# Kernel tuning notes

Measured on AMD Instinct MI355X. Metric: run time of the kernel, lower is better.

The kernel has to match this reference:

```python
import jax, jax.numpy as jnp
import numpy as np

NUM_STUDENTS = 50000
NUM_PROBLEMS = 10000
EMBED_DIM = 64
NNZ = 3200000


def _spmm(rows, cols, vals, x, num_out):
    # out[r] = sum_{edges e with rows[e]==r} vals[e] * x[cols[e]]
    msgs = vals[:, None] * x[cols]  # [nnz, d]
    return jax.ops.segment_sum(msgs, rows, num_segments=num_out)


def setup_inputs() -> dict:
    key = jax.random.key(0)
    ks = jax.random.split(key, 8)
    return {
        "student_embeds": jax.random.normal(ks[0], (NUM_STUDENTS, EMBED_DIM), jnp.float32),
        "problem_embeds": jax.random.normal(ks[1], (NUM_PROBLEMS, EMBED_DIM), jnp.float32),
        "a_rows": jax.random.randint(ks[2], (NNZ,), 0, NUM_STUDENTS, jnp.int32),
        "a_cols": jax.random.randint(ks[3], (NNZ,), 0, NUM_PROBLEMS, jnp.int32),
        "a_vals": jax.random.uniform(ks[4], (NNZ,), jnp.float32),
        "ia_rows": jax.random.randint(ks[5], (NNZ,), 0, NUM_STUDENTS, jnp.int32),
        "ia_cols": jax.random.randint(ks[6], (NNZ,), 0, NUM_PROBLEMS, jnp.int32),
        "ia_vals": jax.random.uniform(ks[7], (NNZ,), jnp.float32),
    }


def reference(student_embeds, problem_embeds, a_rows, a_cols, a_vals,
              ia_rows, ia_cols, ia_vals):
    num_students = student_embeds.shape[0]
    num_problems = problem_embeds.shape[0]
    # a_matrix @ problem_embeds
    student_embeds_c = _spmm(a_rows, a_cols, a_vals, problem_embeds, num_students)
    # a_matrix.T @ student_embeds (swap roles of rows/cols)
    problem_embeds_c = _spmm(a_cols, a_rows, a_vals, student_embeds, num_problems)
    student_embeds_ic = _spmm(ia_rows, ia_cols, ia_vals, problem_embeds, num_students)
    problem_embeds_ic = _spmm(ia_cols, ia_rows, ia_vals, student_embeds, num_problems)
    return (student_embeds_c, student_embeds_ic, problem_embeds_c, problem_embeds_ic)
```

## Files before the change

kernel.cpp:

```cpp
#include <hip/hip_runtime.h>
#include <hip/hip_bf16.h>

#define NBMAX 256
#define TILE  4096
#define KPT   16
#define BINSMAX 512
#define SLP   520

__device__ __forceinline__ int seg8(unsigned r, unsigned mult8) {
    return (int)__umulhi(r, mult8);
}

__global__ __launch_bounds__(256) void hist_all(
        const int* __restrict__ k0, const int* __restrict__ k1,
        const int* __restrict__ k2, const int* __restrict__ k3,
        int* __restrict__ gcnt4, int nnz, int rsh_s, int rsh_p) {
    __shared__ int h[NBMAX];
    int dir = blockIdx.x & 3;
    const int* key = (dir == 0) ? k0 : (dir == 1) ? k1 : (dir == 2) ? k2 : k3;
    int rsh = (dir & 1) ? rsh_p : rsh_s;
    h[threadIdx.x] = 0;
    __syncthreads();
    int ch = blockIdx.x >> 2, nch = gridDim.x >> 2;
    int nnz4 = nnz >> 2;
    for (int i = ch * 256 + threadIdx.x; i < nnz4; i += nch * 256) {
        int4 k4 = ((const int4*)key)[i];
        atomicAdd(&h[k4.x >> rsh], 1);
        atomicAdd(&h[k4.y >> rsh], 1);
        atomicAdd(&h[k4.z >> rsh], 1);
        atomicAdd(&h[k4.w >> rsh], 1);
    }
    if (ch == 0) {
        for (int i = (nnz4 << 2) + threadIdx.x; i < nnz; i += 256)
            atomicAdd(&h[key[i] >> rsh], 1);
    }
    __syncthreads();
    int v = h[threadIdx.x];
    if (v) atomicAdd(&gcnt4[dir * NBMAX + threadIdx.x], v);
}

__global__ __launch_bounds__(256) void scan_all(
        const int* __restrict__ gcnt4, int* __restrict__ boffs4,
        int* __restrict__ bcur4, int nb_s, int nb_p, int nnz,
        int* __restrict__ offsE, int* __restrict__ offsO, int NS, int NP8) {
    __shared__ int tmp[NBMAX];
    int dir = blockIdx.x, tid = threadIdx.x;
    int nb = (dir & 1) ? nb_p : nb_s;
    int v = (tid < nb) ? gcnt4[dir * NBMAX + tid] : 0;
    tmp[tid] = v;
    __syncthreads();
    for (int off = 1; off < NBMAX; off <<= 1) {
        int t = (tid >= off) ? tmp[tid - off] : 0;
        __syncthreads();
        tmp[tid] += t;
        __syncthreads();
    }
    if (tid < nb) {
        int e = tmp[tid] - v;
        boffs4[dir * (NBMAX + 1) + tid] = e;
        bcur4[dir * NBMAX + tid] = e;
    }
    if (tid == 0) boffs4[dir * (NBMAX + 1) + nb] = nnz;
    if (dir == 0 && tid == 0) { offsE[NS] = nnz; offsO[NP8] = nnz; }
}

__global__ __launch_bounds__(256) void staged_scatter(
        const int* __restrict__ key, const int* __restrict__ other,
        const float* __restrict__ vals, int* __restrict__ cursor,
        uint2* __restrict__ edges, int nnz, int rsh) {
    __shared__ int lhist[NBMAX], lofs[NBMAX], lbase[NBMAX];
    __shared__ uint2 stage[TILE];
    __shared__ int   sslot[TILE];
    int tid = threadIdx.x;
    int lmask = (1 << rsh) - 1;
    int ntiles = (nnz + TILE - 1) / TILE;
    for (int tile = blockIdx.x; tile < ntiles; tile += gridDim.x) {
        int tbeg = tile * TILE;
        int n = nnz - tbeg; if (n > TILE) n = TILE;
        lhist[tid] = 0;
        __syncthreads();
        int myb[KPT], myr[KPT]; unsigned myo[KPT]; float myv[KPT];
        #pragma unroll
        for (int g = 0; g < 4; ++g) {
            int s = g * 1024 + tid * 4;
            if (s + 4 <= n) {
                int i = tbeg + s;
                int4   k4 = *(const int4*)(key + i);
                int4   o4 = *(const int4*)(other + i);
                float4 v4 = *(const float4*)(vals + i);
                int   kk[4] = {k4.x, k4.y, k4.z, k4.w};
                int   oo[4] = {o4.x, o4.y, o4.z, o4.w};
                float vv[4] = {v4.x, v4.y, v4.z, v4.w};
                #pragma unroll
                for (int k = 0; k < 4; ++k) {
                    int m = g * 4 + k;
                    myb[m] = kk[k] >> rsh;
                    myo[m] = (unsigned)oo[k] | ((unsigned)(kk[k] & lmask) << 16);
                    myv[m] = vv[k];
                    myr[m] = atomicAdd(&lhist[myb[m]], 1);
                }
            } else {
                #pragma unroll
                for (int k = 0; k < 4; ++k) {
                    int m = g * 4 + k;
                    int s2 = s + k;
                    if (s2 < n) {
                        int i = tbeg + s2;
                        int ky = key[i];
                        myb[m] = ky >> rsh;
                        myo[m] = (unsigned)other[i] | ((unsigned)(ky & lmask) << 16);
                        myv[m] = vals[i];
                        myr[m] = atomicAdd(&lhist[myb[m]], 1);
                    } else myb[m] = -1;
                }
            }
        }
        __syncthreads();
        int h = lhist[tid];
        lofs[tid] = h;
        __syncthreads();
        for (int off = 1; off < NBMAX; off <<= 1) {
            int t = (tid >= off) ? lofs[tid - off] : 0;
            __syncthreads();
            lofs[tid] += t;
            __syncthreads();
        }
        lofs[tid] -= h;
        if (h > 0) lbase[tid] = atomicAdd(&cursor[tid], h);
        __syncthreads();
        #pragma unroll
        for (int k = 0; k < KPT; ++k) {
            if (myb[k] >= 0) {
                int ls = lofs[myb[k]] + myr[k];
                stage[ls] = make_uint2(myo[k], __float_as_uint(myv[k]));
                sslot[ls] = lbase[myb[k]] + myr[k];
            }
        }
        __syncthreads();
        #pragma unroll
        for (int k = 0; k < KPT; ++k) {
            int s = k * 256 + tid;
            if (s < n) edges[sslot[s]] = stage[s];
        }
        __syncthreads();
    }
}

__global__ __launch_bounds__(512) void row_scatter2(
        const uint2* __restrict__ e1, uint2* __restrict__ e2,
        const int* __restrict__ boffs, int* __restrict__ offs,
        int odd, int nb, int rsh, int nrows, unsigned mult8) {
    __shared__ int cnt[8 * SLP];
    __shared__ int tot[512];
    __shared__ int lcur[BINSMAX];
    int tid = threadIdx.x;
    int g = blockIdx.x;
    int x = g & 7;
    int sk = (g >> 3) & 7;
    int bi = g >> 6;
    int b = x + 8 * bi;
    if (b >= nb) return;
    int bins = odd ? (8 << rsh) : (1 << rsh);
    int beg = boffs[b], end = boffs[b + 1];
    int len = end - beg;
    for (int i = tid; i < 8 * SLP; i += 512) cnt[i] = 0;
    __syncthreads();
    int psh = 0;
    {
        int per = (len + 7) >> 3;
        while ((1 << psh) < per) psh++;
    }
    if (len > 0) {
        for (int i = beg + tid; i < end; i += 512) {
            uint2 e = e1[i];
            int lrow = (int)(e.x >> 16);
            int bin = odd ? (lrow * 8 + seg8(e.x & 0xFFFFu, mult8)) : lrow;
            int sl = (i - beg) >> psh;
            atomicAdd(&cnt[sl * SLP + bin], 1);
        }
    }
    __syncthreads();
    int own = 0;
    if (tid < bins) {
        #pragma unroll
        for (int j = 0; j < 8; ++j) own += cnt[j * SLP + tid];
    }
    tot[tid] = (tid < bins) ? own : 0;
    __syncthreads();
    for (int off = 1; off < 512; off <<= 1) {
        int t = (tid >= off) ? tot[tid - off] : 0;
        __syncthreads();
        tot[tid] += t;
        __syncthreads();
    }
    if (tid < bins) {
        int fineoff = tot[tid] - own;
        int basej = 0;
        for (int j = 0; j < sk; ++j) basej += cnt[j * SLP + tid];
        lcur[tid] = beg + fineoff + basej;
        if (sk == 0) {
            if (!odd) {
                int row = (b << rsh) + tid;
                if (row < nrows) offs[row] = beg + fineoff;
            } else {
                int row = (b << rsh) + (tid >> 3);
                if (row < nrows) offs[(row << 3) + (tid & 7)] = beg + fineoff;
            }
        }
    }
    __syncthreads();
    int lo = beg + (sk << psh);
    int hi = lo + (1 << psh); if (hi > end) hi = end;
    for (int i = lo + tid; i < hi; i += 512) {
        uint2 e = e1[i];
        int lrow = (int)(e.x >> 16);
        int bin = odd ? (lrow * 8 + seg8(e.x & 0xFFFFu, mult8)) : lrow;
        int slot = atomicAdd(&lcur[bin], 1);
        e2[slot] = make_uint2(e.x & 0xFFFFu, e.y);
    }
}

__device__ __forceinline__ float4 gather_row4(
        int beg, int end, const uint2* __restrict__ edges,
        const float* __restrict__ x, int lane) {
    int q = lane >> 4, l16 = lane & 15;
    const float* xq = x + (l16 << 2);
    float4 acc = make_float4(0.f, 0.f, 0.f, 0.f);
    for (int base = beg; base < end; base += 64) {
        int n = end - base; if (n > 64) n = 64;
        uint2 e = make_uint2(0u, 0u);
        if (lane < n) e = edges[base + lane];
        int   c0 = __shfl((int)e.x, q);
        float v0 = __uint_as_float(__shfl((int)e.y, q));
        int   c1 = __shfl((int)e.x, 4 + q);
        float v1 = __uint_as_float(__shfl((int)e.y, 4 + q));
        float4 x0 = *(const float4*)(xq + (((size_t)c0) << 6));
        float4 x1 = *(const float4*)(xq + (((size_t)c1) << 6));
        for (int j = 8; j < n; j += 8) {
            int   nc0 = __shfl((int)e.x, j + q);
            float nv0 = __uint_as_float(__shfl((int)e.y, j + q));
            int   nc1 = __shfl((int)e.x, j + 4 + q);
            float nv1 = __uint_as_float(__shfl((int)e.y, j + 4 + q));
            float4 nx0 = *(const float4*)(xq + (((size_t)nc0) << 6));
            float4 nx1 = *(const float4*)(xq + (((size_t)nc1) << 6));
            acc.x += v0 * x0.x; acc.y += v0 * x0.y;
            acc.z += v0 * x0.z; acc.w += v0 * x0.w;
            acc.x += v1 * x1.x; acc.y += v1 * x1.y;
            acc.z += v1 * x1.z; acc.w += v1 * x1.w;
            v0 = nv0; v1 = nv1; x0 = nx0; x1 = nx1;
        }
        acc.x += v0 * x0.x; acc.y += v0 * x0.y;
        acc.z += v0 * x0.z; acc.w += v0 * x0.w;
        acc.x += v1 * x1.x; acc.y += v1 * x1.y;
        acc.z += v1 * x1.z; acc.w += v1 * x1.w;
    }
    acc.x += __shfl_xor(acc.x, 16); acc.y += __shfl_xor(acc.y, 16);
    acc.z += __shfl_xor(acc.z, 16); acc.w += __shfl_xor(acc.w, 16);
    acc.x += __shfl_xor(acc.x, 32); acc.y += __shfl_xor(acc.y, 32);
    acc.z += __shfl_xor(acc.z, 32); acc.w += __shfl_xor(acc.w, 32);
    return acc;
}

__global__ __launch_bounds__(256) void row_gather(
        const int* __restrict__ offs, const uint2* __restrict__ edges,
        const float* __restrict__ x, float* __restrict__ out, int nrows) {
    int r = blockIdx.x * 4 + (threadIdx.x >> 6);
    int lane = threadIdx.x & 63;
    if (r >= nrows) return;
    float4 acc = gather_row4(offs[r], offs[r + 1], edges, x, lane);
    if ((lane >> 4) == 0)
        *(float4*)(out + (((size_t)r) << 6) + ((lane & 15) << 2)) = acc;
}

__global__ __launch_bounds__(256) void xcd_gather(
        const int* __restrict__ offs, const uint2* __restrict__ edges,
        const float* __restrict__ x, float* __restrict__ partial, int NP) {
    int g = blockIdx.x;
    int slot = g & 7;
    int t = g >> 3;
    int wave = threadIdx.x >> 6, lane = threadIdx.x & 63;
    int r = t * 4 + wave;
    if (r >= NP) return;
    int bin = r * 8 + slot;
    float4 acc = gather_row4(offs[bin], offs[bin + 1], edges, x, lane);
    if ((lane >> 4) == 0)
        *(float4*)(partial + (size_t)slot * NP * 64 + (((size_t)r) << 6) + ((lane & 15) << 2)) = acc;
}

__global__ __launch_bounds__(256) void reduce8(
        const float* __restrict__ partial, float* __restrict__ out, int n4) {
    int i = blockIdx.x * 256 + threadIdx.x;
    if (i < n4) {
        const float4* p = (const float4*)partial;
        float4 s = make_float4(0.f, 0.f, 0.f, 0.f);
        #pragma unroll
        for (int xx = 0; xx < 8; ++xx) {
            float4 v = p[(size_t)xx * n4 + i];
            s.x += v.x; s.y += v.y; s.z += v.z; s.w += v.w;
        }
        ((float4*)out)[i] = s;
    }
}

__global__ void spmm_scatter_kernel(const int* __restrict__ rows, const int* __restrict__ cols,
                                    const float* __restrict__ vals,
                                    const float* __restrict__ s_emb, const float* __restrict__ p_emb,
                                    float* __restrict__ out_s, float* __restrict__ out_p, int nnz) {
    long long t = (long long)blockIdx.x * blockDim.x + threadIdx.x;
    int e = (int)(t >> 6);
    int d = (int)(t & 63);
    if (e >= nnz) return;
    int r = rows[e];
    int c = cols[e];
    float v = vals[e];
    atomicAdd(&out_s[(size_t)r * 64 + d], v * p_emb[(size_t)c * 64 + d]);
    atomicAdd(&out_p[(size_t)c * 64 + d], v * s_emb[(size_t)r * 64 + d]);
}

extern "C" void kernel_launch(void* const* d_in, const int* in_sizes, int n_in,
                              void* d_out, int out_size, void* d_ws, size_t ws_size,
                              hipStream_t stream) {
    const float* s_emb   = (const float*)d_in[0];
    const float* p_emb   = (const float*)d_in[1];
    const int*   a_rows  = (const int*)d_in[2];
    const int*   a_cols  = (const int*)d_in[3];
    const float* a_vals  = (const float*)d_in[4];
    const int*   ia_rows = (const int*)d_in[5];
    const int*   ia_cols = (const int*)d_in[6];
    const float* ia_vals = (const float*)d_in[7];

    const int NS  = in_sizes[0] / 64;
    const int NP  = in_sizes[1] / 64;
    const int nnz = in_sizes[2];
    const int NP8 = NP * 8;

    float* out = (float*)d_out;
    float* out_sc  = out;
    float* out_sic = out_sc  + (size_t)NS * 64;
    float* out_pc  = out_sic + (size_t)NS * 64;
    float* out_pic = out_pc  + (size_t)NP * 64;

    int rsh_s = 0; while ((((long long)NS + (1LL << rsh_s) - 1) >> rsh_s) > NBMAX) rsh_s++;
    int rsh_p = 0; while ((((long long)NP + (1LL << rsh_p) - 1) >> rsh_p) > NBMAX) rsh_p++;
    int nb_s = (NS + (1 << rsh_s) - 1) >> rsh_s;
    int nb_p = (NP + (1 << rsh_p) - 1) >> rsh_p;
    unsigned mult8 = (unsigned)((8ULL << 32) / (unsigned)NS);

    const size_t edges_bytes = (size_t)nnz * sizeof(uint2);
    const size_t offsE_bytes = (size_t)(NS + 1) * sizeof(int);
    const size_t offsO_bytes = (size_t)(NP8 + 1) * sizeof(int);
    const size_t need = 2 * edges_bytes + offsE_bytes + offsO_bytes
                      + (size_t)(4 * NBMAX + 4 * (NBMAX + 1) + 4 * NBMAX) * sizeof(int) + 256;
    const bool packable = (NS <= 0xFFFF) && (NP <= 0xFFFF) &&
                          ((1 << rsh_s) <= BINSMAX) && ((8 << rsh_p) <= BINSMAX) &&
                          (edges_bytes >= (size_t)NP8 * 64 * sizeof(float)) &&
                          ((NP * 64) % 4 == 0);

    if (ws_size < need || !packable) {
        hipMemsetAsync(d_out, 0, (size_t)out_size * sizeof(float), stream);
        const long long total = (long long)nnz * 64;
        const int grid = (int)((total + 255) / 256);
        spmm_scatter_kernel<<<grid, 256, 0, stream>>>(a_rows, a_cols, a_vals, s_emb, p_emb,
                                                      out_sc, out_pc, nnz);
        spmm_scatter_kernel<<<grid, 256, 0, stream>>>(ia_rows, ia_cols, ia_vals, s_emb, p_emb,
                                                      out_sic, out_pic, nnz);
        return;
    }

    char* w = (char*)d_ws;
    uint2* edges1 = (uint2*)w;  w += edges_bytes;
    uint2* edges2 = (uint2*)w;  w += edges_bytes;
    int*   offsE  = (int*)w;    w += offsE_bytes;
    int*   offsO  = (int*)w;    w += offsO_bytes;
    int*   gcnt4  = (int*)w;    w += 4 * NBMAX * sizeof(int);
    int*   boffs4 = (int*)w;    w += 4 * (NBMAX + 1) * sizeof(int);
    int*   bcur4  = (int*)w;
    float* partial = (float*)edges1;

    hipMemsetAsync(gcnt4, 0, 4 * NBMAX * sizeof(int), stream);
    hist_all<<<1024, 256, 0, stream>>>(a_rows, a_cols, ia_rows, ia_cols,
                                       gcnt4, nnz, rsh_s, rsh_p);
    scan_all<<<4, 256, 0, stream>>>(gcnt4, boffs4, bcur4, nb_s, nb_p, nnz,
                                    offsE, offsO, NS, NP8);

    const int ntiles = (nnz + TILE - 1) / TILE;
    const int grid_rs_s = 64 * ((nb_s + 7) / 8);
    const int grid_rs_p = 64 * ((nb_p + 7) / 8);

    struct Dir { const int* key; const int* other; const float* vals;
                 float* out; int odd; };
    Dir dirs[4] = {
        { a_rows,  a_cols,  a_vals,  out_sc,  0 },
        { a_cols,  a_rows,  a_vals,  out_pc,  1 },
        { ia_rows, ia_cols, ia_vals, out_sic, 0 },
        { ia_cols, ia_rows, ia_vals, out_pic, 1 },
    };
    for (int t = 0; t < 4; ++t) {
        const Dir& D = dirs[t];
        if (!D.odd) {
            staged_scatter<<<ntiles, 256, 0, stream>>>(D.key, D.other, D.vals,
                                                       bcur4 + t * NBMAX, edges1, nnz, rsh_s);
            row_scatter2<<<grid_rs_s, 512, 0, stream>>>(edges1, edges2,
                                                        boffs4 + t * (NBMAX + 1), offsE,
                                                        0, nb_s, rsh_s, NS, mult8);
            row_gather<<<(NS + 3) / 4, 256, 0, stream>>>(offsE, edges2, p_emb, D.out, NS);
        } else {
            staged_scatter<<<ntiles, 256, 0, stream>>>(D.key, D.other, D.vals,
                                                       bcur4 + t * NBMAX, edges1, nnz, rsh_p);
            row_scatter2<<<grid_rs_p, 512, 0, stream>>>(edges1, edges2,
                                                        boffs4 + t * (NBMAX + 1), offsO,
                                                        1, nb_p, rsh_p, NP, mult8);
            xcd_gather<<<8 * ((NP + 3) / 4), 256, 0, stream>>>(offsO, edges2,
                                                               s_emb, partial, NP);
            reduce8<<<(NP * 64 / 4 + 255) / 256, 256, 0, stream>>>(partial, D.out, NP * 64 / 4);
        }
    }
}
```

Before: 620.5 us.

## Split row scatter into separate bin-count and bin-scatter kernels

Previously, each of the 8 sub-blocks of a bucket re-read the entire bucket's edges to build per-slice histograms, so edges were read redundantly 8 times for counting. Now a bin_count kernel has each sub-block count only its own slice and write the counts to a global buffer. A second kernel, bin_scatter, reads the 8 slice counts per bin, scans them and scatters the edges. This removes the redundant reads but adds an extra launch and a global count buffer round trip. The XCD-aware block index mapping is also dropped in favour of a plain b*8+sk layout.

```diff
diff --git a/kernel.cpp b/kernel.cpp
--- a/kernel.cpp
+++ b/kernel.cpp
@@ -5,7 +5,6 @@
 #define TILE  4096
 #define KPT   16
 #define BINSMAX 512
-#define SLP   520
 
 __device__ __forceinline__ int seg8(unsigned r, unsigned mult8) {
     return (int)__umulhi(r, mult8);
@@ -146,44 +145,56 @@
     }
 }
 
-__global__ __launch_bounds__(512) void row_scatter2(
+__global__ __launch_bounds__(512) void bin_count(
+        const uint2* __restrict__ e1, const int* __restrict__ boffs,
+        int* __restrict__ cnt_g, int odd, int nb, int rsh, unsigned mult8) {
+    __shared__ int cnt[BINSMAX];
+    int tid = threadIdx.x;
+    int g = blockIdx.x;
+    int sk = g & 7;
+    int b = g >> 3;
+    if (b >= nb) return;
+    int bins = odd ? (8 << rsh) : (1 << rsh);
+    int beg = boffs[b], end = boffs[b + 1];
+    int len = end - beg;
+    if (tid < bins) cnt[tid] = 0;
+    __syncthreads();
+    int psh = 0;
+    { int per = (len + 7) >> 3; while ((1 << psh) < per) psh++; }
+    int lo = beg + (sk << psh);
+    int hi = lo + (1 << psh); if (hi > end) hi = end;
+    for (int i = lo + tid; i < hi; i += 512) {
+        uint2 e = e1[i];
+        int lrow = (int)(e.x >> 16);
+        int bin = odd ? (lrow * 8 + seg8(e.x & 0xFFFFu, mult8)) : lrow;
+        atomicAdd(&cnt[bin], 1);
+    }
+    __syncthreads();
+    if (tid < bins) cnt_g[g * BINSMAX + tid] = cnt[tid];
+}
+
+__global__ __launch_bounds__(512) void bin_scatter(
         const uint2* __restrict__ e1, uint2* __restrict__ e2,
-        const int* __restrict__ boffs, int* __restrict__ offs,
-        int odd, int nb, int rsh, int nrows, unsigned mult8) {
-    __shared__ int cnt[8 * SLP];
+        const int* __restrict__ boffs, const int* __restrict__ cnt_g,
+        int* __restrict__ offs, int odd, int nb, int rsh, int nrows,
+        unsigned mult8) {
     __shared__ int tot[512];
     __shared__ int lcur[BINSMAX];
     int tid = threadIdx.x;
     int g = blockIdx.x;
-    int x = g & 7;
-    int sk = (g >> 3) & 7;
-    int bi = g >> 6;
-    int b = x + 8 * bi;
+    int sk = g & 7;
+    int b = g >> 3;
     if (b >= nb) return;
     int bins = odd ? (8 << rsh) : (1 << rsh);
     int beg = boffs[b], end = boffs[b + 1];
     int len = end - beg;
-    for (int i = tid; i < 8 * SLP; i += 512) cnt[i] = 0;
-    __syncthreads();
-    int psh = 0;
-    {
-        int per = (len + 7) >> 3;
-        while ((1 << psh) < per) psh++;
-    }
-    if (len > 0) {
-        for (int i = beg + tid; i < end; i += 512) {
-            uint2 e = e1[i];
-            int lrow = (int)(e.x >> 16);
-            int bin = odd ? (lrow * 8 + seg8(e.x & 0xFFFFu, mult8)) : lrow;
-            int sl = (i - beg) >> psh;
-            atomicAdd(&cnt[sl * SLP + bin], 1);
-        }
-    }
-    __syncthreads();
-    int own = 0;
+    int c[8]; int own = 0;
     if (tid < bins) {
         #pragma unroll
-        for (int j = 0; j < 8; ++j) own += cnt[j * SLP + tid];
+        for (int j = 0; j < 8; ++j) {
+            c[j] = cnt_g[(b * 8 + j) * BINSMAX + tid];
+            own += c[j];
+        }
     }
     tot[tid] = (tid < bins) ? own : 0;
     __syncthreads();
@@ -196,7 +207,8 @@
     if (tid < bins) {
         int fineoff = tot[tid] - own;
         int basej = 0;
-        for (int j = 0; j < sk; ++j) basej += cnt[j * SLP + tid];
+        #pragma unroll
+        for (int j = 0; j < 8; ++j) if (j < sk) basej += c[j];
         lcur[tid] = beg + fineoff + basej;
         if (sk == 0) {
             if (!odd) {
@@ -209,6 +221,8 @@
         }
     }
     __syncthreads();
+    int psh = 0;
+    { int per = (len + 7) >> 3; while ((1 << psh) < per) psh++; }
     int lo = beg + (sk << psh);
     int hi = lo + (1 << psh); if (hi > end) hi = end;
     for (int i = lo + tid; i < hi; i += 512) {
@@ -349,7 +363,8 @@
     const size_t edges_bytes = (size_t)nnz * sizeof(uint2);
     const size_t offsE_bytes = (size_t)(NS + 1) * sizeof(int);
     const size_t offsO_bytes = (size_t)(NP8 + 1) * sizeof(int);
-    const size_t need = 2 * edges_bytes + offsE_bytes + offsO_bytes
+    const size_t cntg_bytes  = (size_t)NBMAX * 8 * BINSMAX * sizeof(int);
+    const size_t need = 2 * edges_bytes + offsE_bytes + offsO_bytes + cntg_bytes
                       + (size_t)(4 * NBMAX + 4 * (NBMAX + 1) + 4 * NBMAX) * sizeof(int) + 256;
     const bool packable = (NS <= 0xFFFF) && (NP <= 0xFFFF) &&
                           ((1 << rsh_s) <= BINSMAX) && ((8 << rsh_p) <= BINSMAX) &&
@@ -374,7 +389,8 @@
     int*   offsO  = (int*)w;    w += offsO_bytes;
     int*   gcnt4  = (int*)w;    w += 4 * NBMAX * sizeof(int);
     int*   boffs4 = (int*)w;    w += 4 * (NBMAX + 1) * sizeof(int);
-    int*   bcur4  = (int*)w;
+    int*   bcur4  = (int*)w;    w += 4 * NBMAX * sizeof(int);
+    int*   cnt_g  = (int*)w;
     float* partial = (float*)edges1;
 
     hipMemsetAsync(gcnt4, 0, 4 * NBMAX * sizeof(int), stream);
@@ -384,8 +400,6 @@
                                     offsE, offsO, NS, NP8);
 
     const int ntiles = (nnz + TILE - 1) / TILE;
-    const int grid_rs_s = 64 * ((nb_s + 7) / 8);
-    const int grid_rs_p = 64 * ((nb_p + 7) / 8);
 
     struct Dir { const int* key; const int* other; const float* vals;
                  float* out; int odd; };
@@ -400,16 +414,20 @@
         if (!D.odd) {
             staged_scatter<<<ntiles, 256, 0, stream>>>(D.key, D.other, D.vals,
                                                        bcur4 + t * NBMAX, edges1, nnz, rsh_s);
-            row_scatter2<<<grid_rs_s, 512, 0, stream>>>(edges1, edges2,
-                                                        boffs4 + t * (NBMAX + 1), offsE,
-                                                        0, nb_s, rsh_s, NS, mult8);
+            bin_count<<<nb_s * 8, 512, 0, stream>>>(edges1, boffs4 + t * (NBMAX + 1),
+                                                    cnt_g, 0, nb_s, rsh_s, mult8);
+            bin_scatter<<<nb_s * 8, 512, 0, stream>>>(edges1, edges2,
+                                                      boffs4 + t * (NBMAX + 1), cnt_g, offsE,
+                                                      0, nb_s, rsh_s, NS, mult8);
             row_gather<<<(NS + 3) / 4, 256, 0, stream>>>(offsE, edges2, p_emb, D.out, NS);
         } else {
             staged_scatter<<<ntiles, 256, 0, stream>>>(D.key, D.other, D.vals,
                                                        bcur4 + t * NBMAX, edges1, nnz, rsh_p);
-            row_scatter2<<<grid_rs_p, 512, 0, stream>>>(edges1, edges2,
-                                                        boffs4 + t * (NBMAX + 1), offsO,
-                                                        1, nb_p, rsh_p, NP, mult8);
+            bin_count<<<nb_p * 8, 512, 0, stream>>>(edges1, boffs4 + t * (NBMAX + 1),
+                                                    cnt_g, 1, nb_p, rsh_p, mult8);
+            bin_scatter<<<nb_p * 8, 512, 0, stream>>>(edges1, edges2,
+                                                      boffs4 + t * (NBMAX + 1), cnt_g, offsO,
+                                                      1, nb_p, rsh_p, NP, mult8);
             xcd_gather<<<8 * ((NP + 3) / 4), 256, 0, stream>>>(offsO, edges2,
                                                                s_emb, partial, NP);
             reduce8<<<(NP * 64 / 4 + 255) / 256, 256, 0, stream>>>(partial, D.out, NP * 64 / 4);
```

Result: no change. 631.3 us (+1.7%).
